# Kernel tuning notes

Measured on AMD Instinct MI355X. Metric: run time of the kernel, lower is better.

## Reference

```python
import jax, jax.numpy as jnp
import numpy as np

BATCH = 8192
INPUT_SIZE = 64
OUTPUT_SIZE = 16384  # 128x128 SOM grid


def setup_inputs() -> dict:
    key = jax.random.key(0)
    kx, kw = jax.random.split(key)
    x = jax.random.normal(kx, (BATCH, INPUT_SIZE), dtype=jnp.float32)
    # Xavier-normal * 1e-4 as in the torch init; plain scaled normal is fine for a baseline
    xavier_std = float(np.sqrt(2.0 / (INPUT_SIZE + OUTPUT_SIZE)))
    weights = 1e-4 * xavier_std * jax.random.normal(kw, (INPUT_SIZE, OUTPUT_SIZE), dtype=jnp.float32)
    return {"x": x, "weights": weights}


def reference(x, weights):
    # Squared Euclidean distance between each input row and each codebook column.
    # Same math as ||w[None,:, :] - x[:, :, None]||^2 summed over the feature dim,
    x2 = jnp.sum(x * x, axis=1, keepdims=True)          # (B, 1)
    w2 = jnp.sum(weights * weights, axis=0)[None, :]    # (1, N)
    cross = jnp.einsum('bd,dn->bn', x, weights)         # (B, N)
    norms2 = x2 + w2 - 2.0 * cross                      # (B, N)
    return norms2
```

## Files before the change

### kernel.cpp

```cpp
#include <hip/hip_runtime.h>
#include <hip/hip_bf16.h>

#define BATCH 8192
#define IN_D  64
#define OUT_N 16384

typedef __attribute__((ext_vector_type(8)))  short bf16x8;
typedef __attribute__((ext_vector_type(16))) float f32x16;
typedef __attribute__((ext_vector_type(4)))  float f32x4;

static constexpr size_t WT_OFF  = 0;
static constexpr size_t XB_OFF  = WT_OFF + (size_t)OUT_N * IN_D * 2;
static constexpr size_t X2_OFF  = XB_OFF + (size_t)BATCH * IN_D * 2;
static constexpr size_t W2_OFF  = X2_OFF + (size_t)BATCH * 4;
static constexpr size_t WS_NEED = W2_OFF + (size_t)OUT_N * 4;

__global__ void prep_x(const float* __restrict__ x, __hip_bfloat16* __restrict__ xb,
                       float* __restrict__ x2) {
    const int t   = threadIdx.x;
    const int row = blockIdx.x * 16 + (t >> 4);
    const int kq  = t & 15;
    const f32x4 v = *reinterpret_cast<const f32x4*>(x + (size_t)row * IN_D + kq * 4);
    float s = v[0]*v[0] + v[1]*v[1] + v[2]*v[2] + v[3]*v[3];
    s += __shfl_xor(s, 1);
    s += __shfl_xor(s, 2);
    s += __shfl_xor(s, 4);
    s += __shfl_xor(s, 8);
    if (kq == 0) x2[row] = s;
    union { __hip_bfloat16 h[4]; ushort4 u; } cvt;
    cvt.h[0] = __float2bfloat16(v[0]);
    cvt.h[1] = __float2bfloat16(v[1]);
    cvt.h[2] = __float2bfloat16(v[2]);
    cvt.h[3] = __float2bfloat16(v[3]);
    *reinterpret_cast<ushort4*>(&xb[(size_t)row * IN_D + kq * 4]) = cvt.u;
}

__global__ void prep_w(const float* __restrict__ w, __hip_bfloat16* __restrict__ wt,
                       float* __restrict__ w2) {
    __shared__ float tile[64][65];
    const int t  = threadIdx.x;
    const int n0 = blockIdx.x * 64;
    #pragma unroll
    for (int i = 0; i < 4; ++i) {
        int p = i * 256 + t;
        int d = p >> 4, nq = p & 15;
        const f32x4 v = *reinterpret_cast<const f32x4*>(w + (size_t)d * OUT_N + n0 + nq * 4);
        tile[d][nq*4+0] = v[0]; tile[d][nq*4+1] = v[1];
        tile[d][nq*4+2] = v[2]; tile[d][nq*4+3] = v[3];
    }
    __syncthreads();
    if (t < 64) {
        float s = 0.f;
        #pragma unroll
        for (int d = 0; d < 64; ++d) { float f = tile[d][t]; s += f * f; }
        w2[n0 + t] = s;
    }
    #pragma unroll
    for (int i = 0; i < 4; ++i) {
        int c = i * 256 + t;
        int n = c >> 4, kq = c & 15;
        union { __hip_bfloat16 h[4]; ushort4 u; } cvt;
        #pragma unroll
        for (int j = 0; j < 4; ++j) cvt.h[j] = __float2bfloat16(tile[kq*4+j][n]);
        *reinterpret_cast<ushort4*>(&wt[(size_t)(n0 + n) * IN_D + kq * 4]) = cvt.u;
    }
}

__global__ __launch_bounds__(256, 2) void som_gemm(
    const __hip_bfloat16* __restrict__ xb, const __hip_bfloat16* __restrict__ wt,
    const float* __restrict__ x2, const float* __restrict__ w2,
    float* __restrict__ out) {
    const int lane = threadIdx.x & 63;
    const int wv   = threadIdx.x >> 6;
    const int m0   = blockIdx.y * 128 + (wv >> 1) * 64;
    const int n0   = blockIdx.x * 128 + (wv & 1) * 64;
    const int l31  = lane & 31, l5 = lane >> 5;

    bf16x8 a[2][4], b[2][4];
    #pragma unroll
    for (int mi = 0; mi < 2; ++mi) {
        const __hip_bfloat16* base = xb + (size_t)(m0 + mi * 32 + l31) * IN_D + l5 * 8;
        #pragma unroll
        for (int ks = 0; ks < 4; ++ks)
            a[mi][ks] = *reinterpret_cast<const bf16x8*>(base + ks * 16);
    }
    #pragma unroll
    for (int ni = 0; ni < 2; ++ni) {
        const __hip_bfloat16* base = wt + (size_t)(n0 + ni * 32 + l31) * IN_D + l5 * 8;
        #pragma unroll
        for (int ks = 0; ks < 4; ++ks)
            b[ni][ks] = *reinterpret_cast<const bf16x8*>(base + ks * 16);
    }

    f32x16 acc[2][2] = {};
    #pragma unroll
    for (int ks = 0; ks < 4; ++ks)
        #pragma unroll
        for (int mi = 0; mi < 2; ++mi)
            #pragma unroll
            for (int ni = 0; ni < 2; ++ni)
                acc[mi][ni] = __builtin_amdgcn_mfma_f32_32x32x16_bf16(
                    a[mi][ks], b[ni][ks], acc[mi][ni], 0, 0, 0);

    #pragma unroll
    for (int ni = 0; ni < 2; ++ni) {
        const float w2v = w2[n0 + ni * 32 + l31];
        const size_t colOff = (size_t)(n0 + ni * 32 + l31);
        #pragma unroll
        for (int mi = 0; mi < 2; ++mi) {
            const int rbase = m0 + mi * 32 + 4 * l5;
            #pragma unroll
            for (int rg = 0; rg < 4; ++rg) {
                const f32x4 xv = *reinterpret_cast<const f32x4*>(x2 + rbase + 8 * rg);
                #pragma unroll
                for (int j = 0; j < 4; ++j) {
                    const int row = rbase + 8 * rg + j;
                    __builtin_nontemporal_store(
                        xv[j] + w2v - 2.0f * acc[mi][ni][4 * rg + j],
                        out + (size_t)row * OUT_N + colOff);
                }
            }
        }
    }
}

__global__ void som_fallback(const float* __restrict__ x, const float* __restrict__ w,
                             float* __restrict__ out) {
    __shared__ float xs[16][64];
    const int t  = threadIdx.x;
    const int m0 = blockIdx.y * 16;
    const int n0 = blockIdx.x * 256;
    {
        int row = t >> 4, kq = t & 15;
        const f32x4 v = *reinterpret_cast<const f32x4*>(x + (size_t)(m0 + row) * IN_D + kq * 4);
        xs[row][kq*4+0] = v[0]; xs[row][kq*4+1] = v[1];
        xs[row][kq*4+2] = v[2]; xs[row][kq*4+3] = v[3];
    }
    __syncthreads();
    const int col = n0 + t;
    float acc[16];
    #pragma unroll
    for (int r = 0; r < 16; ++r) acc[r] = 0.f;
    for (int d = 0; d < 64; ++d) {
        const float wv = w[(size_t)d * OUT_N + col];
        #pragma unroll
        for (int r = 0; r < 16; ++r) { float df = xs[r][d] - wv; acc[r] += df * df; }
    }
    #pragma unroll
    for (int r = 0; r < 16; ++r)
        __builtin_nontemporal_store(acc[r], out + (size_t)(m0 + r) * OUT_N + col);
}

extern "C" void kernel_launch(void* const* d_in, const int* in_sizes, int n_in,
                              void* d_out, int out_size, void* d_ws, size_t ws_size,
                              hipStream_t stream) {
    const float* x = (const float*)d_in[0];
    const float* w = (const float*)d_in[1];
    float* out = (float*)d_out;

    if (ws_size >= WS_NEED) {
        char* ws = (char*)d_ws;
        __hip_bfloat16* wt = (__hip_bfloat16*)(ws + WT_OFF);
        __hip_bfloat16* xb = (__hip_bfloat16*)(ws + XB_OFF);
        float* x2 = (float*)(ws + X2_OFF);
        float* w2 = (float*)(ws + W2_OFF);
        prep_x<<<BATCH / 16, 256, 0, stream>>>(x, xb, x2);
        prep_w<<<OUT_N / 64, 256, 0, stream>>>(w, wt, w2);
        dim3 grid(OUT_N / 128, BATCH / 128);
        som_gemm<<<grid, 256, 0, stream>>>(xb, wt, x2, w2, out);
    } else {
        dim3 grid(OUT_N / 256, BATCH / 16);
        som_fallback<<<grid, 256, 0, stream>>>(x, w, out);
    }
}
```

Before: 121.1 us.

## Merge prep kernels and halve GEMM tile height for higher occupancy

```diff
diff --git a/kernel.cpp b/kernel.cpp
--- a/kernel.cpp
+++ b/kernel.cpp
@@ -15,74 +15,72 @@
 static constexpr size_t W2_OFF  = X2_OFF + (size_t)BATCH * 4;
 static constexpr size_t WS_NEED = W2_OFF + (size_t)OUT_N * 4;
 
-__global__ void prep_x(const float* __restrict__ x, __hip_bfloat16* __restrict__ xb,
-                       float* __restrict__ x2) {
-    const int t   = threadIdx.x;
-    const int row = blockIdx.x * 16 + (t >> 4);
-    const int kq  = t & 15;
-    const f32x4 v = *reinterpret_cast<const f32x4*>(x + (size_t)row * IN_D + kq * 4);
-    float s = v[0]*v[0] + v[1]*v[1] + v[2]*v[2] + v[3]*v[3];
-    s += __shfl_xor(s, 1);
-    s += __shfl_xor(s, 2);
-    s += __shfl_xor(s, 4);
-    s += __shfl_xor(s, 8);
-    if (kq == 0) x2[row] = s;
-    union { __hip_bfloat16 h[4]; ushort4 u; } cvt;
-    cvt.h[0] = __float2bfloat16(v[0]);
-    cvt.h[1] = __float2bfloat16(v[1]);
-    cvt.h[2] = __float2bfloat16(v[2]);
-    cvt.h[3] = __float2bfloat16(v[3]);
-    *reinterpret_cast<ushort4*>(&xb[(size_t)row * IN_D + kq * 4]) = cvt.u;
-}
-
-__global__ void prep_w(const float* __restrict__ w, __hip_bfloat16* __restrict__ wt,
-                       float* __restrict__ w2) {
-    __shared__ float tile[64][65];
-    const int t  = threadIdx.x;
-    const int n0 = blockIdx.x * 64;
-    #pragma unroll
-    for (int i = 0; i < 4; ++i) {
-        int p = i * 256 + t;
-        int d = p >> 4, nq = p & 15;
-        const f32x4 v = *reinterpret_cast<const f32x4*>(w + (size_t)d * OUT_N + n0 + nq * 4);
-        tile[d][nq*4+0] = v[0]; tile[d][nq*4+1] = v[1];
-        tile[d][nq*4+2] = v[2]; tile[d][nq*4+3] = v[3];
-    }
-    __syncthreads();
-    if (t < 64) {
-        float s = 0.f;
+__global__ void prep_all(const float* __restrict__ x, const float* __restrict__ w,
+                         __hip_bfloat16* __restrict__ xb, float* __restrict__ x2,
+                         __hip_bfloat16* __restrict__ wt, float* __restrict__ w2) {
+    const int t = threadIdx.x;
+    if (blockIdx.x < 512) {
+        const int row = blockIdx.x * 16 + (t >> 4);
+        const int kq  = t & 15;
+        const f32x4 v = *reinterpret_cast<const f32x4*>(x + (size_t)row * IN_D + kq * 4);
+        float s = v[0]*v[0] + v[1]*v[1] + v[2]*v[2] + v[3]*v[3];
+        s += __shfl_xor(s, 1);
+        s += __shfl_xor(s, 2);
+        s += __shfl_xor(s, 4);
+        s += __shfl_xor(s, 8);
+        if (kq == 0) x2[row] = s;
+        union { __hip_bfloat16 h[4]; ushort4 u; } cvt;
+        cvt.h[0] = __float2bfloat16(v[0]);
+        cvt.h[1] = __float2bfloat16(v[1]);
+        cvt.h[2] = __float2bfloat16(v[2]);
+        cvt.h[3] = __float2bfloat16(v[3]);
+        *reinterpret_cast<ushort4*>(&xb[(size_t)row * IN_D + kq * 4]) = cvt.u;
+    } else {
+        __shared__ float tile[64][65];
+        const int n0 = (blockIdx.x - 512) * 64;
         #pragma unroll
-        for (int d = 0; d < 64; ++d) { float f = tile[d][t]; s += f * f; }
-        w2[n0 + t] = s;
-    }
-    #pragma unroll
-    for (int i = 0; i < 4; ++i) {
-        int c = i * 256 + t;
-        int n = c >> 4, kq = c & 15;
-        union { __hip_bfloat16 h[4]; ushort4 u; } cvt;
+        for (int i = 0; i < 4; ++i) {
+            int p = i * 256 + t;
+            int d = p >> 4, nq = p & 15;
+            const f32x4 v = *reinterpret_cast<const f32x4*>(w + (size_t)d * OUT_N + n0 + nq * 4);
+            tile[d][nq*4+0] = v[0]; tile[d][nq*4+1] = v[1];
+            tile[d][nq*4+2] = v[2]; tile[d][nq*4+3] = v[3];
+        }
+        __syncthreads();
+        if (t < 64) {
+            float s = 0.f;
+            #pragma unroll
+            for (int d = 0; d < 64; ++d) { float f = tile[d][t]; s += f * f; }
+            w2[n0 + t] = s;
+        }
         #pragma unroll
-        for (int j = 0; j < 4; ++j) cvt.h[j] = __float2bfloat16(tile[kq*4+j][n]);
-        *reinterpret_cast<ushort4*>(&wt[(size_t)(n0 + n) * IN_D + kq * 4]) = cvt.u;
+        for (int i = 0; i < 4; ++i) {
+            int c = i * 256 + t;
+            int n = c >> 4, kq = c & 15;
+            union { __hip_bfloat16 h[4]; ushort4 u; } cvt;
+            #pragma unroll
+            for (int j = 0; j < 4; ++j) cvt.h[j] = __float2bfloat16(tile[kq*4+j][n]);
+            *reinterpret_cast<ushort4*>(&wt[(size_t)(n0 + n) * IN_D + kq * 4]) = cvt.u;
+        }
     }
 }
 
-__global__ __launch_bounds__(256, 2) void som_gemm(
+__global__ __launch_bounds__(256, 4) void som_gemm(
     const __hip_bfloat16* __restrict__ xb, const __hip_bfloat16* __restrict__ wt,
     const float* __restrict__ x2, const float* __restrict__ w2,
     float* __restrict__ out) {
     const int lane = threadIdx.x & 63;
     const int wv   = threadIdx.x >> 6;
-    const int m0   = blockIdx.y * 128 + (wv >> 1) * 64;
+    const int m0   = blockIdx.y * 64 + (wv >> 1) * 32;
     const int n0   = blockIdx.x * 128 + (wv & 1) * 64;
     const int l31  = lane & 31, l5 = lane >> 5;
 
-    bf16x8 a[2][4], b[2][4];
-    #pragma unroll
-    for (int mi = 0; mi < 2; ++mi) {
-        const __hip_bfloat16* base = xb + (size_t)(m0 + mi * 32 + l31) * IN_D + l5 * 8;
+    bf16x8 a[4], b[2][4];
+    {
+        const __hip_bfloat16* base = xb + (size_t)(m0 + l31) * IN_D + l5 * 8;
         #pragma unroll
         for (int ks = 0; ks < 4; ++ks)
-            a[mi][ks] = *reinterpret_cast<const bf16x8*>(base + ks * 16);
+            a[ks] = *reinterpret_cast<const bf16x8*>(base + ks * 16);
     }
     #pragma unroll
     for (int ni = 0; ni < 2; ++ni) {
@@ -92,34 +90,26 @@
             b[ni][ks] = *reinterpret_cast<const bf16x8*>(base + ks * 16);
     }
 
-    f32x16 acc[2][2] = {};
+    f32x16 acc[2] = {};
     #pragma unroll
     for (int ks = 0; ks < 4; ++ks)
         #pragma unroll
-        for (int mi = 0; mi < 2; ++mi)
-            #pragma unroll
-            for (int ni = 0; ni < 2; ++ni)
-                acc[mi][ni] = __builtin_amdgcn_mfma_f32_32x32x16_bf16(
-                    a[mi][ks], b[ni][ks], acc[mi][ni], 0, 0, 0);
+        for (int ni = 0; ni < 2; ++ni)
+            acc[ni] = __builtin_amdgcn_mfma_f32_32x32x16_bf16(a[ks], b[ni][ks], acc[ni], 0, 0, 0);
 
+    const float w2v0 = w2[n0 + l31];
+    const float w2v1 = w2[n0 + 32 + l31];
+    const int rbase = m0 + 4 * l5;
+    float* const obase = out + l31;
     #pragma unroll
-    for (int ni = 0; ni < 2; ++ni) {
-        const float w2v = w2[n0 + ni * 32 + l31];
-        const size_t colOff = (size_t)(n0 + ni * 32 + l31);
+    for (int rg = 0; rg < 4; ++rg) {
+        const f32x4 xv = *reinterpret_cast<const f32x4*>(x2 + rbase + 8 * rg);
         #pragma unroll
-        for (int mi = 0; mi < 2; ++mi) {
-            const int rbase = m0 + mi * 32 + 4 * l5;
-            #pragma unroll
-            for (int rg = 0; rg < 4; ++rg) {
-                const f32x4 xv = *reinterpret_cast<const f32x4*>(x2 + rbase + 8 * rg);
-                #pragma unroll
-                for (int j = 0; j < 4; ++j) {
-                    const int row = rbase + 8 * rg + j;
-                    __builtin_nontemporal_store(
-                        xv[j] + w2v - 2.0f * acc[mi][ni][4 * rg + j],
-                        out + (size_t)row * OUT_N + colOff);
-                }
-            }
+        for (int j = 0; j < 4; ++j) {
+            const int row = rbase + 8 * rg + j;
+            float* const orow = obase + (size_t)row * OUT_N + n0;
+            __builtin_nontemporal_store(xv[j] + w2v0 - 2.0f * acc[0][4 * rg + j], orow);
+            __builtin_nontemporal_store(xv[j] + w2v1 - 2.0f * acc[1][4 * rg + j], orow + 32);
         }
     }
 }
@@ -164,9 +154,8 @@
         __hip_bfloat16* xb = (__hip_bfloat16*)(ws + XB_OFF);
         float* x2 = (float*)(ws + X2_OFF);
         float* w2 = (float*)(ws + W2_OFF);
-        prep_x<<<BATCH / 16, 256, 0, stream>>>(x, xb, x2);
-        prep_w<<<OUT_N / 64, 256, 0, stream>>>(w, wt, w2);
-        dim3 grid(OUT_N / 128, BATCH / 128);
+        prep_all<<<512 + 256, 256, 0, stream>>>(x, w, xb, x2, wt, w2);
+        dim3 grid(OUT_N / 128, BATCH / 64);
         som_gemm<<<grid, 256, 0, stream>>>(xb, wt, x2, w2, out);
     } else {
         dim3 grid(OUT_N / 256, BATCH / 16);
```

Result: slower. 126.7 us (+4.6%).
